# Optimization experiments

Hardware: AMD Instinct MI355X
Metric: run time of the kernel (lower is better)

## Reference

```python
import jax, jax.numpy as jnp
import numpy as np

N_IMAGE, N_CAPTION, N_REGION, N_WORD = 128, 32, 36, 24
EMBED, NUM_BLOCK, N_KERNELS, HID, OUT = 1024, 32, 8, 64, 1
BLOCK = EMBED // NUM_BLOCK  # 32
LAMBDA = 4.0
EPS = 1e-8


def l2norm(x, axis):
    # matches torch l2norm: x / (sqrt(sum(x^2)) + eps)
    return x / (jnp.sqrt(jnp.sum(x * x, axis=axis, keepdims=True)) + EPS)


def wn_linear(x, v, g, b):
    # torch weight_norm(Linear): W = g * v / ||v||_row
    w = v * (g / jnp.linalg.norm(v, axis=1))[:, None]
    return x @ w.T + b


def setup_inputs() -> dict:
    key = jax.random.key(0)
    ks = jax.random.split(key, 12)
    return {
        'images': jax.random.normal(ks[0], (N_IMAGE, N_REGION, EMBED), jnp.float32),
        'captions': jax.random.normal(ks[1], (N_CAPTION, N_WORD, EMBED), jnp.float32),
        'depends': jax.random.randint(ks[2], (N_CAPTION, N_WORD - 1, 2), 0, N_WORD, jnp.int32),
        'cap_lens': jnp.full((N_CAPTION,), N_WORD, jnp.int32),
        'mean_k': jax.random.normal(ks[3], (N_KERNELS,), jnp.float32) * 0.1,
        'prec_k': 1.0 + jax.random.normal(ks[4], (N_KERNELS,), jnp.float32) * 0.1,
        'conv_w': jax.random.normal(ks[5], (N_KERNELS, NUM_BLOCK, HID // N_KERNELS), jnp.float32) * 0.05,
        'out1_v': jax.random.normal(ks[6], (HID, HID), jnp.float32) * 0.05,
        'out1_g': jnp.ones((HID,), jnp.float32),
        'out1_b': jnp.zeros((HID,), jnp.float32),
        'out2_v': jax.random.normal(ks[7], (OUT, HID), jnp.float32) * 0.05,
        'out2_g': jnp.ones((OUT,), jnp.float32),
        'out2_b': jnp.zeros((OUT,), jnp.float32),
    }


def reference(images, captions, depends, cap_lens, mean_k, prec_k, conv_w,
              out1_v, out1_g, out1_b, out2_v, out2_g, out2_b):
    B = images.shape[0]

    def per_caption(cap, dep):
        # cap: (nw, d); dep: (n_dep, 2)
        # --- intra_relations: softmax(Q K^T * lambda) ---
        words_sim = jax.nn.softmax((cap @ cap.T) * LAMBDA, axis=-1)  # (nw, nw)
        # --- build_sparse_graph: symmetric adjacency, pair 0 skipped, + eye ---
        valid = jnp.arange(dep.shape[0]) > 0
        r = jnp.where(valid, dep[:, 0], N_WORD)  # dump invalid into pad row
        c = jnp.where(valid, dep[:, 1], N_WORD)
        adj = jnp.zeros((N_WORD + 1, N_WORD + 1), images.dtype)
        adj = adj.at[r, c].max(1.0)
        adj = adj.at[c, r].max(1.0)
        adj = adj[:N_WORD, :N_WORD] + jnp.eye(N_WORD, dtype=images.dtype)
        # --- node_level_matching: inter_relations + weighted context ---
        attn = jnp.einsum('brd,wd->brw', images, cap)          # (B, R, nw)
        attn = jax.nn.leaky_relu(attn, 0.1)
        attn = l2norm(attn, axis=2)
        attn = jax.nn.softmax(jnp.swapaxes(attn, 1, 2) * LAMBDA, axis=-1)  # (B, nw, R)
        wctx = jnp.einsum('bwr,brd->bwd', attn, images)        # (B, nw, d)
        # block-wise cosine similarity
        q = cap.reshape(N_WORD, NUM_BLOCK, BLOCK)              # (nw, nb, blk)
        ctx = wctx.reshape(B, N_WORD, NUM_BLOCK, BLOCK)        # (B, nw, nb, blk)
        num = jnp.einsum('wkc,nwkc->nwk', q, ctx)
        qn = jnp.linalg.norm(q, axis=-1)                       # (nw, nb)
        cn = jnp.linalg.norm(ctx, axis=-1)                     # (B, nw, nb)
        tnode = num / jnp.maximum(qn[None] * cn, EPS)          # (B, nw, nb)
        # --- structure_level_matching (sparse path) ---
        nb_feat = adj[None, :, :, None] * tnode[:, :, None, :]  # (B, nw, nw, nb)
        nb_w = l2norm(adj * words_sim, axis=1)                  # (nw, nw) neighbor-normalized
        # Gaussian kernel weights of the graph convolution
        diff = (nb_w[..., None] - mean_k) ** 2                  # (nw, nw, nk)
        kw = jnp.exp(-0.5 * diff / (1e-14 + prec_k ** 2))
        kw = kw / jnp.sum(kw, axis=-1, keepdims=True)
        # aggregate neighbors per kernel, then per-kernel linear, concat
        agg = jnp.einsum('ijk,nijf->nikf', kw, nb_feat)         # (B, nw, nk, nb)
        hidden = jnp.einsum('nikf,kfo->niko', agg, conv_w).reshape(B * N_WORD, HID)
        h = jnp.tanh(wn_linear(hidden, out1_v, out1_g, out1_b))
        s = wn_linear(h, out2_v, out2_g, out2_b)                # (B*nw, 1)
        return s.reshape(B, -1).mean(axis=1)                    # (B,)

    sims = jax.vmap(per_caption)(captions, depends)             # (n_caption, B)
    return sims.T                                               # (B, n_caption)
```

## Files before the change

### kernel.cpp

```cpp
#include <hip/hip_runtime.h>
#include <math.h>

#define N_IMAGE   128
#define N_CAPTION 32
#define N_REGION  36
#define N_WORD    24
#define EMBED     1024
#define EPSV      1e-8f

#define WS_W1 0
#define WS_W2 4096
#define WS_S  4160
#define WS_QN 10304

__global__ __launch_bounds__(64) void prep_weights_k(
    const float* __restrict__ v1, const float* __restrict__ g1,
    const float* __restrict__ v2, const float* __restrict__ g2,
    float* __restrict__ ws) {
  const int j = threadIdx.x;
  float s = 0.f;
  for (int c0 = 0; c0 < 64; c0++) { float x = v1[j * 64 + c0]; s += x * x; }
  const float sc = g1[j] / sqrtf(s);
  for (int c0 = 0; c0 < 64; c0++) ws[WS_W1 + j * 64 + c0] = v1[j * 64 + c0] * sc;
  float s2 = 0.f;
  for (int c0 = 0; c0 < 64; c0++) { float x = v2[c0]; s2 += x * x; }
  ws[WS_W2 + j] = v2[j] * (g2[0] / sqrtf(s2));
}

__global__ __launch_bounds__(256) void cap_prep_k(
    const float* __restrict__ captions, const int* __restrict__ depends,
    const float* __restrict__ mean_k, const float* __restrict__ prec_k,
    float* __restrict__ ws) {
  __shared__ __align__(16) float capT[24][132];
  __shared__ float partB[2304];
  __shared__ float wsL[24][25];
  __shared__ float adjL[24][24];

  const int c = blockIdx.x, tid = threadIdx.x;
  const float* capC = captions + c * N_WORD * EMBED;

  const int g = tid / 36, t = tid % 36;
  const int i0 = (t / 6) * 4, j0 = (t % 6) * 4;
  const bool act = tid < 144;
  float acc[4][4] = {};
  for (int k0 = 0; k0 < EMBED; k0 += 128) {
    for (int idx = tid; idx < 24 * 32; idx += 256) {
      int r = idx >> 5, q = idx & 31;
      *(float4*)&capT[r][q * 4] = *(const float4*)(capC + r * EMBED + k0 + q * 4);
    }
    __syncthreads();
    if (act) {
#pragma unroll
      for (int q8 = 0; q8 < 8; q8++) {
        const int q = g * 8 + q8;
        float4 av[4], bv[4];
#pragma unroll
        for (int a = 0; a < 4; a++) av[a] = *(const float4*)&capT[i0 + a][q * 4];
#pragma unroll
        for (int b = 0; b < 4; b++) bv[b] = *(const float4*)&capT[j0 + b][q * 4];
#pragma unroll
        for (int a = 0; a < 4; a++)
#pragma unroll
          for (int b = 0; b < 4; b++)
            acc[a][b] += av[a].x * bv[b].x + av[a].y * bv[b].y +
                         av[a].z * bv[b].z + av[a].w * bv[b].w;
      }
    }
    __syncthreads();
  }
  if (act)
#pragma unroll
    for (int a = 0; a < 4; a++)
#pragma unroll
      for (int b = 0; b < 4; b++)
        partB[g * 576 + (i0 + a) * 24 + (j0 + b)] = acc[a][b];
  __syncthreads();
  for (int p = tid; p < 576; p += 256)
    wsL[p / 24][p % 24] = partB[p] + partB[p + 576] + partB[p + 1152] + partB[p + 1728];
  {
    float* ap = &adjL[0][0];
    for (int p = tid; p < 576; p += 256) ap[p] = 0.f;
  }
  __syncthreads();
  if (tid < 24) {
    const int i = tid;
    float m = -1e30f;
    for (int j = 0; j < 24; j++) m = fmaxf(m, wsL[i][j]);
    float ssum = 0.f;
    for (int j = 0; j < 24; j++) {
      float e = expf(4.0f * (wsL[i][j] - m));
      wsL[i][j] = e; ssum += e;
    }
    float inv = 1.0f / ssum;
    for (int j = 0; j < 24; j++) wsL[i][j] *= inv;
  }
  __syncthreads();
  if (tid >= 1 && tid < 23) {
    int r = depends[c * 46 + tid * 2];
    int cc = depends[c * 46 + tid * 2 + 1];
    if ((unsigned)r < 24u && (unsigned)cc < 24u) {
      adjL[r][cc] = 1.f;
      adjL[cc][r] = 1.f;
    }
  }
  __syncthreads();
  if (tid < 24) adjL[tid][tid] += 1.f;
  __syncthreads();
  if (tid < 24) {
    const int i = tid;
    float mk[8], pk2[8];
#pragma unroll
    for (int k = 0; k < 8; k++) {
      mk[k] = mean_k[k];
      float p = prec_k[k];
      pk2[k] = 1e-14f + p * p;
    }
    float s2 = 0.f;
    for (int j = 0; j < 24; j++) {
      float a = adjL[i][j] * wsL[i][j];
      s2 += a * a;
    }
    const float inv = 1.0f / (sqrtf(s2) + EPSV);
    float accS[8] = {};
    for (int j = 0; j < 24; j++) {
      const float adj_ij = adjL[i][j];
      if (adj_ij != 0.f) {
        const float nb = adj_ij * wsL[i][j] * inv;
        float wk[8], ssum = 0.f;
#pragma unroll
        for (int k = 0; k < 8; k++) {
          float d = nb - mk[k];
          wk[k] = expf(-0.5f * d * d / pk2[k]);
          ssum += wk[k];
        }
        const float invs = adj_ij / ssum;
#pragma unroll
        for (int k = 0; k < 8; k++) accS[k] += wk[k] * invs;
      }
    }
#pragma unroll
    for (int k = 0; k < 8; k++) ws[WS_S + (c * 24 + i) * 8 + k] = accS[k];
  }
  for (int p = tid; p < 768; p += 256) {
    const int w = p >> 5, f = p & 31;
    const float* q = capC + w * EMBED + f * 32;
    float s = 0.f;
#pragma unroll
    for (int d = 0; d < 32; d += 4) {
      float4 v = *(const float4*)(q + d);
      s += v.x * v.x + v.y * v.y + v.z * v.z + v.w * v.w;
    }
    ws[WS_QN + (c * 24 + w) * 32 + f] = sqrtf(s);
  }
}

__global__ __launch_bounds__(256) void main_k(
    const float* __restrict__ images, const float* __restrict__ captions,
    const float* __restrict__ conv_w, const float* __restrict__ out1_b,
    const float* __restrict__ out2_b, const float* __restrict__ ws,
    float* __restrict__ out) {
  __shared__ __align__(16) float imgT[36][132];
  __shared__ __align__(16) float capT[24][132];
  __shared__ float attnL[36][25];
  __shared__ __align__(16) float attnT[36][28];
  __shared__ __align__(16) float ctxL[24][132];
  __shared__ float tnodeL[24][33];
  __shared__ __align__(16) float hiddenL[24][72];
  __shared__ float sred[24];

  const int tid = threadIdx.x;
  const int bid = blockIdx.x;
  const int n = bid >> 5, c = bid & 31;
  const float* imgN = images + n * N_REGION * EMBED;
  const float* capC = captions + c * N_WORD * EMBED;

  const int g1 = tid / 54, t1 = tid % 54;
  const int r0 = (t1 / 6) * 4, w0s1 = (t1 % 6) * 4;
  const bool act1 = tid < 216;
  float acc1[4][4] = {};

  for (int k0 = 0; k0 < EMBED; k0 += 128) {
    for (int idx = tid; idx < 36 * 32; idx += 256) {
      int r = idx >> 5, q = idx & 31;
      *(float4*)&imgT[r][q * 4] = *(const float4*)(imgN + r * EMBED + k0 + q * 4);
    }
    for (int idx = tid; idx < 24 * 32; idx += 256) {
      int r = idx >> 5, q = idx & 31;
      *(float4*)&capT[r][q * 4] = *(const float4*)(capC + r * EMBED + k0 + q * 4);
    }
    __syncthreads();
    if (act1) {
#pragma unroll
      for (int q8 = 0; q8 < 8; q8++) {
        const int q = g1 * 8 + q8;
        float4 av[4], bv[4];
#pragma unroll
        for (int a = 0; a < 4; a++) av[a] = *(const float4*)&imgT[r0 + a][q * 4];
#pragma unroll
        for (int b = 0; b < 4; b++) bv[b] = *(const float4*)&capT[w0s1 + b][q * 4];
#pragma unroll
        for (int a = 0; a < 4; a++)
#pragma unroll
          for (int b = 0; b < 4; b++)
            acc1[a][b] += av[a].x * bv[b].x + av[a].y * bv[b].y +
                          av[a].z * bv[b].z + av[a].w * bv[b].w;
      }
    }
    __syncthreads();
  }
  {
    float* part = &imgT[0][0];
    if (act1) {
#pragma unroll
      for (int a = 0; a < 4; a++)
#pragma unroll
        for (int b = 0; b < 4; b++)
          part[g1 * 864 + (r0 + a) * 24 + (w0s1 + b)] = acc1[a][b];
    }
    __syncthreads();
    for (int p = tid; p < 864; p += 256) {
      float s = part[p] + part[p + 864] + part[p + 1728] + part[p + 2592];
      attnL[p / 24][p % 24] = (s > 0.f) ? s : 0.1f * s;
    }
    __syncthreads();
  }

  if (tid < 36) {
    const int r = tid;
    float s = 0.f;
    for (int w = 0; w < 24; w++) { float x = attnL[r][w]; s += x * x; }
    const float inv = 1.f / (sqrtf(s) + EPSV);
    for (int w = 0; w < 24; w++) attnL[r][w] *= inv;
  }
  __syncthreads();
  if (tid < 24) {
    const int w = tid;
    float m = -1e30f;
    for (int r = 0; r < 36; r++) m = fmaxf(m, attnL[r][w]);
    float ssum = 0.f;
    for (int r = 0; r < 36; r++) {
      float e = expf(4.0f * (attnL[r][w] - m));
      attnT[r][w] = e; ssum += e;
    }
    const float inv = 1.0f / ssum;
    for (int r = 0; r < 36; r++) attnT[r][w] *= inv;
  }
  __syncthreads();

  for (int k0 = 0; k0 < EMBED; k0 += 128) {
    for (int idx = tid; idx < 36 * 32; idx += 256) {
      int r = idx >> 5, q = idx & 31;
      *(float4*)&imgT[r][q * 4] = *(const float4*)(imgN + r * EMBED + k0 + q * 4);
    }
    for (int idx = tid; idx < 24 * 32; idx += 256) {
      int r = idx >> 5, q = idx & 31;
      *(float4*)&capT[r][q * 4] = *(const float4*)(capC + r * EMBED + k0 + q * 4);
    }
    __syncthreads();
    if (tid < 192) {
      const int w0 = (tid >> 5) * 4, dq = tid & 31;
      float4 a0 = make_float4(0.f, 0.f, 0.f, 0.f), a1 = a0, a2 = a0, a3 = a0;
      for (int r = 0; r < 36; r++) {
        float4 iv = *(const float4*)&imgT[r][dq * 4];
        float4 aw = *(const float4*)&attnT[r][w0];
        a0.x += aw.x * iv.x; a0.y += aw.x * iv.y; a0.z += aw.x * iv.z; a0.w += aw.x * iv.w;
        a1.x += aw.y * iv.x; a1.y += aw.y * iv.y; a1.z += aw.y * iv.z; a1.w += aw.y * iv.w;
        a2.x += aw.z * iv.x; a2.y += aw.z * iv.y; a2.z += aw.z * iv.z; a2.w += aw.z * iv.w;
        a3.x += aw.w * iv.x; a3.y += aw.w * iv.y; a3.z += aw.w * iv.z; a3.w += aw.w * iv.w;
      }
      *(float4*)&ctxL[w0 + 0][dq * 4] = a0;
      *(float4*)&ctxL[w0 + 1][dq * 4] = a1;
      *(float4*)&ctxL[w0 + 2][dq * 4] = a2;
      *(float4*)&ctxL[w0 + 3][dq * 4] = a3;
    }
    __syncthreads();
    if (tid < 96) {
      const int w = tid >> 2, fl = tid & 3;
      float num = 0.f, cn2 = 0.f;
#pragma unroll
      for (int d = 0; d < 32; d += 4) {
        float4 cv = *(const float4*)&ctxL[w][fl * 32 + d];
        float4 qv = *(const float4*)&capT[w][fl * 32 + d];
        num += qv.x * cv.x + qv.y * cv.y + qv.z * cv.z + qv.w * cv.w;
        cn2 += cv.x * cv.x + cv.y * cv.y + cv.z * cv.z + cv.w * cv.w;
      }
      const int f = (k0 >> 5) + fl;
      const float qn = ws[WS_QN + (c * 24 + w) * 32 + f];
      tnodeL[w][f] = num / fmaxf(qn * sqrtf(cn2), EPSV);
    }
    __syncthreads();
  }

  float* W1t = &imgT[0][0];
  float* w2s = &capT[0][0];
  float* b1s = &capT[1][0];
  float* Ss  = &attnT[0][0];
  for (int idx = tid; idx < 4096; idx += 256) {
    const int j = idx >> 6, col = idx & 63;
    W1t[col * 68 + j] = ws[WS_W1 + idx];
  }
  for (int p = tid; p < 192; p += 256) Ss[p] = ws[WS_S + c * 192 + p];
  if (tid < 64) w2s[tid] = ws[WS_W2 + tid];
  else if (tid < 128) b1s[tid - 64] = out1_b[tid - 64];
  __syncthreads();

  for (int p = tid; p < 1536; p += 256) {
    const int w = p >> 6, col = p & 63, k = col >> 3, o = col & 7;
    const float* cw = conv_w + k * 256 + o;
    float tacc = 0.f;
#pragma unroll
    for (int f = 0; f < 32; f++) tacc += tnodeL[w][f] * cw[f * 8];
    hiddenL[w][col] = Ss[w * 8 + k] * tacc;
  }
  __syncthreads();

  float hv[2][4];
  {
    int pc = 0;
    for (int p = tid; p < 384; p += 256, pc++) {
      const int w = p >> 4, j0 = (p & 15) * 4;
      float ax = b1s[j0 + 0], ay = b1s[j0 + 1], az = b1s[j0 + 2], aww = b1s[j0 + 3];
      for (int col = 0; col < 64; col += 4) {
        float4 h4 = *(const float4*)&hiddenL[w][col];
        float4 wv0 = *(const float4*)&W1t[(col + 0) * 68 + j0];
        float4 wv1 = *(const float4*)&W1t[(col + 1) * 68 + j0];
        float4 wv2 = *(const float4*)&W1t[(col + 2) * 68 + j0];
        float4 wv3 = *(const float4*)&W1t[(col + 3) * 68 + j0];
        ax  += h4.x * wv0.x + h4.y * wv1.x + h4.z * wv2.x + h4.w * wv3.x;
        ay  += h4.x * wv0.y + h4.y * wv1.y + h4.z * wv2.y + h4.w * wv3.y;
        az  += h4.x * wv0.z + h4.y * wv1.z + h4.z * wv2.z + h4.w * wv3.z;
        aww += h4.x * wv0.w + h4.y * wv1.w + h4.z * wv2.w + h4.w * wv3.w;
      }
      hv[pc][0] = tanhf(ax); hv[pc][1] = tanhf(ay);
      hv[pc][2] = tanhf(az); hv[pc][3] = tanhf(aww);
    }
    __syncthreads();
    pc = 0;
    for (int p = tid; p < 384; p += 256, pc++) {
      const int w = p >> 4, j0 = (p & 15) * 4;
      hiddenL[w][j0 + 0] = hv[pc][0]; hiddenL[w][j0 + 1] = hv[pc][1];
      hiddenL[w][j0 + 2] = hv[pc][2]; hiddenL[w][j0 + 3] = hv[pc][3];
    }
    __syncthreads();
  }

  if (tid < 24) {
    const int w = tid;
    float sv = out2_b[0];
    for (int j = 0; j < 64; j++) sv += hiddenL[w][j] * w2s[j];
    sred[w] = sv;
  }
  __syncthreads();
  if (tid == 0) {
    float s = 0.f;
    for (int w = 0; w < 24; w++) s += sred[w];
    out[n * 32 + c] = s * (1.0f / 24.0f);
  }
}

extern "C" void kernel_launch(void* const* d_in, const int* in_sizes, int n_in,
                              void* d_out, int out_size, void* d_ws, size_t ws_size,
                              hipStream_t stream) {
  const float* images   = (const float*)d_in[0];
  const float* captions = (const float*)d_in[1];
  const int*   depends  = (const int*)d_in[2];
  const float* mean_k   = (const float*)d_in[4];
  const float* prec_k   = (const float*)d_in[5];
  const float* conv_w   = (const float*)d_in[6];
  const float* out1_v   = (const float*)d_in[7];
  const float* out1_g   = (const float*)d_in[8];
  const float* out1_b   = (const float*)d_in[9];
  const float* out2_v   = (const float*)d_in[10];
  const float* out2_g   = (const float*)d_in[11];
  const float* out2_b   = (const float*)d_in[12];
  float* ws  = (float*)d_ws;
  float* out = (float*)d_out;

  prep_weights_k<<<dim3(1), dim3(64), 0, stream>>>(out1_v, out1_g, out2_v, out2_g, ws);
  cap_prep_k<<<dim3(32), dim3(256), 0, stream>>>(captions, depends, mean_k, prec_k, ws);
  main_k<<<dim3(N_IMAGE * N_CAPTION), dim3(256), 0, stream>>>(
      images, captions, conv_w, out1_b, out2_b, ws, out);
}
```

Before: 1.065 ms.

## Shrink main kernel LDS footprint, halve K-chunks, fuse weight prep into cap kernel

```diff
diff --git a/kernel.cpp b/kernel.cpp
--- a/kernel.cpp
+++ b/kernel.cpp
@@ -13,30 +13,37 @@
 #define WS_S  4160
 #define WS_QN 10304
 
-__global__ __launch_bounds__(64) void prep_weights_k(
-    const float* __restrict__ v1, const float* __restrict__ g1,
-    const float* __restrict__ v2, const float* __restrict__ g2,
-    float* __restrict__ ws) {
-  const int j = threadIdx.x;
-  float s = 0.f;
-  for (int c0 = 0; c0 < 64; c0++) { float x = v1[j * 64 + c0]; s += x * x; }
-  const float sc = g1[j] / sqrtf(s);
-  for (int c0 = 0; c0 < 64; c0++) ws[WS_W1 + j * 64 + c0] = v1[j * 64 + c0] * sc;
-  float s2 = 0.f;
-  for (int c0 = 0; c0 < 64; c0++) { float x = v2[c0]; s2 += x * x; }
-  ws[WS_W2 + j] = v2[j] * (g2[0] / sqrtf(s2));
-}
-
 __global__ __launch_bounds__(256) void cap_prep_k(
     const float* __restrict__ captions, const int* __restrict__ depends,
     const float* __restrict__ mean_k, const float* __restrict__ prec_k,
+    const float* __restrict__ v1, const float* __restrict__ g1v,
+    const float* __restrict__ v2, const float* __restrict__ g2v,
     float* __restrict__ ws) {
   __shared__ __align__(16) float capT[24][132];
   __shared__ float partB[2304];
   __shared__ float wsL[24][25];
   __shared__ float adjL[24][24];
 
-  const int c = blockIdx.x, tid = threadIdx.x;
+  const int tid = threadIdx.x;
+
+  if (blockIdx.x == 32) {
+    if (tid < 64) {
+      const int j = tid;
+      float s = 0.f;
+      for (int c0 = 0; c0 < 64; c0 += 4) {
+        float4 x = *(const float4*)(v1 + j * 64 + c0);
+        s += x.x * x.x + x.y * x.y + x.z * x.z + x.w * x.w;
+      }
+      const float sc = g1v[j] / sqrtf(s);
+      for (int c0 = 0; c0 < 64; c0++) ws[WS_W1 + j * 64 + c0] = v1[j * 64 + c0] * sc;
+      float s2 = 0.f;
+      for (int c0 = 0; c0 < 64; c0++) { float x = v2[c0]; s2 += x * x; }
+      ws[WS_W2 + j] = v2[j] * (g2v[0] / sqrtf(s2));
+    }
+    return;
+  }
+
+  const int c = blockIdx.x;
   const float* capC = captions + c * N_WORD * EMBED;
 
   const int g = tid / 36, t = tid % 36;
@@ -154,72 +161,77 @@
   }
 }
 
-__global__ __launch_bounds__(256) void main_k(
+__device__ __forceinline__ void stage_chunk(const float* __restrict__ imgN,
+                                            const float* __restrict__ capC,
+                                            float* IMG, float* CAP,
+                                            int k0, int tid) {
+  for (int idx = tid; idx < 960; idx += 256) {
+    if (idx < 576) {
+      const int r = idx >> 4, q = idx & 15;
+      *(float4*)&IMG[r * 68 + q * 4] = *(const float4*)(imgN + r * EMBED + k0 + q * 4);
+    } else {
+      const int j = idx - 576, r = j >> 4, q = j & 15;
+      *(float4*)&CAP[r * 68 + q * 4] = *(const float4*)(capC + r * EMBED + k0 + q * 4);
+    }
+  }
+}
+
+__global__ __launch_bounds__(256, 4) void main_k(
     const float* __restrict__ images, const float* __restrict__ captions,
     const float* __restrict__ conv_w, const float* __restrict__ out1_b,
     const float* __restrict__ out2_b, const float* __restrict__ ws,
     float* __restrict__ out) {
-  __shared__ __align__(16) float imgT[36][132];
-  __shared__ __align__(16) float capT[24][132];
-  __shared__ float attnL[36][25];
-  __shared__ __align__(16) float attnT[36][28];
-  __shared__ __align__(16) float ctxL[24][132];
-  __shared__ float tnodeL[24][33];
-  __shared__ __align__(16) float hiddenL[24][72];
-  __shared__ float sred[24];
+  __shared__ __align__(16) float bufA[4352];
+  __shared__ __align__(16) float bufB[3648];
+  __shared__ __align__(16) float attnL[36][25];
+  __shared__ float smallb[352];
 
   const int tid = threadIdx.x;
-  const int bid = blockIdx.x;
-  const int n = bid >> 5, c = bid & 31;
+  const int n = blockIdx.x >> 5, c = blockIdx.x & 31;
   const float* imgN = images + n * N_REGION * EMBED;
   const float* capC = captions + c * N_WORD * EMBED;
+  float* IMG = bufA;
+  float* CAP = bufA + 2448;
 
   const int g1 = tid / 54, t1 = tid % 54;
-  const int r0 = (t1 / 6) * 4, w0s1 = (t1 % 6) * 4;
+  const int r0 = (t1 / 6) * 4, w0 = (t1 % 6) * 4;
   const bool act1 = tid < 216;
-  float acc1[4][4] = {};
-
-  for (int k0 = 0; k0 < EMBED; k0 += 128) {
-    for (int idx = tid; idx < 36 * 32; idx += 256) {
-      int r = idx >> 5, q = idx & 31;
-      *(float4*)&imgT[r][q * 4] = *(const float4*)(imgN + r * EMBED + k0 + q * 4);
-    }
-    for (int idx = tid; idx < 24 * 32; idx += 256) {
-      int r = idx >> 5, q = idx & 31;
-      *(float4*)&capT[r][q * 4] = *(const float4*)(capC + r * EMBED + k0 + q * 4);
-    }
+  float acc[4][4] = {};
+  for (int k0 = 0; k0 < EMBED; k0 += 64) {
+    __syncthreads();
+    stage_chunk(imgN, capC, IMG, CAP, k0, tid);
     __syncthreads();
     if (act1) {
 #pragma unroll
-      for (int q8 = 0; q8 < 8; q8++) {
-        const int q = g1 * 8 + q8;
+      for (int qi = 0; qi < 4; qi++) {
+        const int q = g1 * 4 + qi;
         float4 av[4], bv[4];
 #pragma unroll
-        for (int a = 0; a < 4; a++) av[a] = *(const float4*)&imgT[r0 + a][q * 4];
-#pragma unroll
-        for (int b = 0; b < 4; b++) bv[b] = *(const float4*)&capT[w0s1 + b][q * 4];
+        for (int a = 0; a < 4; a++) av[a] = *(const float4*)&IMG[(r0 + a) * 68 + q * 4];
+#pragma unroll
+        for (int b = 0; b < 4; b++) bv[b] = *(const float4*)&CAP[(w0 + b) * 68 + q * 4];
 #pragma unroll
         for (int a = 0; a < 4; a++)
 #pragma unroll
           for (int b = 0; b < 4; b++)
-            acc1[a][b] += av[a].x * bv[b].x + av[a].y * bv[b].y +
-                          av[a].z * bv[b].z + av[a].w * bv[b].w;
-      }
-    }
-    __syncthreads();
-  }
+            acc[a][b] += av[a].x * bv[b].x + av[a].y * bv[b].y +
+                         av[a].z * bv[b].z + av[a].w * bv[b].w;
+      }
+    }
+  }
+  __syncthreads();
   {
-    float* part = &imgT[0][0];
+    float* partB = bufB;
     if (act1) {
 #pragma unroll
       for (int a = 0; a < 4; a++)
 #pragma unroll
         for (int b = 0; b < 4; b++)
-          part[g1 * 864 + (r0 + a) * 24 + (w0s1 + b)] = acc1[a][b];
+          partB[g1 * 864 + (r0 + a) * 24 + (w0 + b)] = acc[a][b];
     }
     __syncthreads();
     for (int p = tid; p < 864; p += 256) {
-      float s = part[p] + part[p + 864] + part[p + 1728] + part[p + 2592];
+      float s = partB[p] + partB[p + 864] + partB[p + 1728] + partB[p + 2592];
       attnL[p / 24][p % 24] = (s > 0.f) ? s : 0.1f * s;
     }
     __syncthreads();
@@ -233,6 +245,7 @@
     for (int w = 0; w < 24; w++) attnL[r][w] *= inv;
   }
   __syncthreads();
+  float* attnW = bufB;
   if (tid < 24) {
     const int w = tid;
     float m = -1e30f;
@@ -240,80 +253,121 @@
     float ssum = 0.f;
     for (int r = 0; r < 36; r++) {
       float e = expf(4.0f * (attnL[r][w] - m));
-      attnT[r][w] = e; ssum += e;
+      attnW[w * 44 + r] = e; ssum += e;
     }
     const float inv = 1.0f / ssum;
-    for (int r = 0; r < 36; r++) attnT[r][w] *= inv;
-  }
-  __syncthreads();
-
-  for (int k0 = 0; k0 < EMBED; k0 += 128) {
-    for (int idx = tid; idx < 36 * 32; idx += 256) {
-      int r = idx >> 5, q = idx & 31;
-      *(float4*)&imgT[r][q * 4] = *(const float4*)(imgN + r * EMBED + k0 + q * 4);
-    }
-    for (int idx = tid; idx < 24 * 32; idx += 256) {
-      int r = idx >> 5, q = idx & 31;
-      *(float4*)&capT[r][q * 4] = *(const float4*)(capC + r * EMBED + k0 + q * 4);
-    }
-    __syncthreads();
-    if (tid < 192) {
-      const int w0 = (tid >> 5) * 4, dq = tid & 31;
-      float4 a0 = make_float4(0.f, 0.f, 0.f, 0.f), a1 = a0, a2 = a0, a3 = a0;
-      for (int r = 0; r < 36; r++) {
-        float4 iv = *(const float4*)&imgT[r][dq * 4];
-        float4 aw = *(const float4*)&attnT[r][w0];
-        a0.x += aw.x * iv.x; a0.y += aw.x * iv.y; a0.z += aw.x * iv.z; a0.w += aw.x * iv.w;
-        a1.x += aw.y * iv.x; a1.y += aw.y * iv.y; a1.z += aw.y * iv.z; a1.w += aw.y * iv.w;
-        a2.x += aw.z * iv.x; a2.y += aw.z * iv.y; a2.z += aw.z * iv.z; a2.w += aw.z * iv.w;
-        a3.x += aw.w * iv.x; a3.y += aw.w * iv.y; a3.z += aw.w * iv.z; a3.w += aw.w * iv.w;
-      }
-      *(float4*)&ctxL[w0 + 0][dq * 4] = a0;
-      *(float4*)&ctxL[w0 + 1][dq * 4] = a1;
-      *(float4*)&ctxL[w0 + 2][dq * 4] = a2;
-      *(float4*)&ctxL[w0 + 3][dq * 4] = a3;
-    }
+    for (int r = 0; r < 36; r++) attnW[w * 44 + r] *= inv;
+  }
+  __syncthreads();
+  float* qnL = &attnL[0][0];
+  for (int p = tid; p < 768; p += 256) qnL[p] = ws[WS_QN + c * 768 + p];
+
+  float* tnodeL = bufB + 1056;
+  const int g3 = tid >> 4, q4 = tid & 15, w03 = g3 * 4;
+  for (int k0 = 0; k0 < EMBED; k0 += 64) {
+    __syncthreads();
+    stage_chunk(imgN, capC, IMG, CAP, k0, tid);
     __syncthreads();
     if (tid < 96) {
-      const int w = tid >> 2, fl = tid & 3;
-      float num = 0.f, cn2 = 0.f;
-#pragma unroll
-      for (int d = 0; d < 32; d += 4) {
-        float4 cv = *(const float4*)&ctxL[w][fl * 32 + d];
-        float4 qv = *(const float4*)&capT[w][fl * 32 + d];
-        num += qv.x * cv.x + qv.y * cv.y + qv.z * cv.z + qv.w * cv.w;
-        cn2 += cv.x * cv.x + cv.y * cv.y + cv.z * cv.z + cv.w * cv.w;
-      }
-      const int f = (k0 >> 5) + fl;
-      const float qn = ws[WS_QN + (c * 24 + w) * 32 + f];
-      tnodeL[w][f] = num / fmaxf(qn * sqrtf(cn2), EPSV);
-    }
-    __syncthreads();
-  }
-
-  float* W1t = &imgT[0][0];
-  float* w2s = &capT[0][0];
-  float* b1s = &capT[1][0];
-  float* Ss  = &attnT[0][0];
+      float4 ctx0 = make_float4(0.f, 0.f, 0.f, 0.f), ctx1 = ctx0, ctx2 = ctx0, ctx3 = ctx0;
+      for (int rb = 0; rb < 36; rb += 4) {
+        float4 iv0 = *(const float4*)&IMG[(rb + 0) * 68 + q4 * 4];
+        float4 iv1 = *(const float4*)&IMG[(rb + 1) * 68 + q4 * 4];
+        float4 iv2 = *(const float4*)&IMG[(rb + 2) * 68 + q4 * 4];
+        float4 iv3 = *(const float4*)&IMG[(rb + 3) * 68 + q4 * 4];
+        float4 a0 = *(const float4*)&attnW[(w03 + 0) * 44 + rb];
+        float4 a1 = *(const float4*)&attnW[(w03 + 1) * 44 + rb];
+        float4 a2 = *(const float4*)&attnW[(w03 + 2) * 44 + rb];
+        float4 a3 = *(const float4*)&attnW[(w03 + 3) * 44 + rb];
+        ctx0.x += a0.x * iv0.x + a0.y * iv1.x + a0.z * iv2.x + a0.w * iv3.x;
+        ctx0.y += a0.x * iv0.y + a0.y * iv1.y + a0.z * iv2.y + a0.w * iv3.y;
+        ctx0.z += a0.x * iv0.z + a0.y * iv1.z + a0.z * iv2.z + a0.w * iv3.z;
+        ctx0.w += a0.x * iv0.w + a0.y * iv1.w + a0.z * iv2.w + a0.w * iv3.w;
+        ctx1.x += a1.x * iv0.x + a1.y * iv1.x + a1.z * iv2.x + a1.w * iv3.x;
+        ctx1.y += a1.x * iv0.y + a1.y * iv1.y + a1.z * iv2.y + a1.w * iv3.y;
+        ctx1.z += a1.x * iv0.z + a1.y * iv1.z + a1.z * iv2.z + a1.w * iv3.z;
+        ctx1.w += a1.x * iv0.w + a1.y * iv1.w + a1.z * iv2.w + a1.w * iv3.w;
+        ctx2.x += a2.x * iv0.x + a2.y * iv1.x + a2.z * iv2.x + a2.w * iv3.x;
+        ctx2.y += a2.x * iv0.y + a2.y * iv1.y + a2.z * iv2.y + a2.w * iv3.y;
+        ctx2.z += a2.x * iv0.z + a2.y * iv1.z + a2.z * iv2.z + a2.w * iv3.z;
+        ctx2.w += a2.x * iv0.w + a2.y * iv1.w + a2.z * iv2.w + a2.w * iv3.w;
+        ctx3.x += a3.x * iv0.x + a3.y * iv1.x + a3.z * iv2.x + a3.w * iv3.x;
+        ctx3.y += a3.x * iv0.y + a3.y * iv1.y + a3.z * iv2.y + a3.w * iv3.y;
+        ctx3.z += a3.x * iv0.z + a3.y * iv1.z + a3.z * iv2.z + a3.w * iv3.z;
+        ctx3.w += a3.x * iv0.w + a3.y * iv1.w + a3.z * iv2.w + a3.w * iv3.w;
+      }
+      float red[8];
+      {
+        float4 c4;
+        c4 = *(const float4*)&CAP[(w03 + 0) * 68 + q4 * 4];
+        red[0] = c4.x * ctx0.x + c4.y * ctx0.y + c4.z * ctx0.z + c4.w * ctx0.w;
+        red[4] = ctx0.x * ctx0.x + ctx0.y * ctx0.y + ctx0.z * ctx0.z + ctx0.w * ctx0.w;
+        c4 = *(const float4*)&CAP[(w03 + 1) * 68 + q4 * 4];
+        red[1] = c4.x * ctx1.x + c4.y * ctx1.y + c4.z * ctx1.z + c4.w * ctx1.w;
+        red[5] = ctx1.x * ctx1.x + ctx1.y * ctx1.y + ctx1.z * ctx1.z + ctx1.w * ctx1.w;
+        c4 = *(const float4*)&CAP[(w03 + 2) * 68 + q4 * 4];
+        red[2] = c4.x * ctx2.x + c4.y * ctx2.y + c4.z * ctx2.z + c4.w * ctx2.w;
+        red[6] = ctx2.x * ctx2.x + ctx2.y * ctx2.y + ctx2.z * ctx2.z + ctx2.w * ctx2.w;
+        c4 = *(const float4*)&CAP[(w03 + 3) * 68 + q4 * 4];
+        red[3] = c4.x * ctx3.x + c4.y * ctx3.y + c4.z * ctx3.z + c4.w * ctx3.w;
+        red[7] = ctx3.x * ctx3.x + ctx3.y * ctx3.y + ctx3.z * ctx3.z + ctx3.w * ctx3.w;
+      }
+#pragma unroll
+      for (int m = 1; m < 8; m <<= 1) {
+#pragma unroll
+        for (int t = 0; t < 8; t++) red[t] += __shfl_xor(red[t], m);
+      }
+      if ((q4 & 7) == 0) {
+        const int f = (k0 >> 5) + (q4 >> 3);
+#pragma unroll
+        for (int j = 0; j < 4; j++) {
+          const float qn = qnL[(w03 + j) * 32 + f];
+          tnodeL[(w03 + j) * 36 + f] = red[j] / fmaxf(qn * sqrtf(red[4 + j]), EPSV);
+        }
+      }
+    }
+  }
+  __syncthreads();
+
+  float* convT = bufA;
+  for (int idx = tid; idx < 2048; idx += 256) {
+    const int f = idx >> 6, col = idx & 63;
+    convT[f * 68 + col] = conv_w[(col >> 3) * 256 + f * 8 + (col & 7)];
+  }
+  float* w2s = smallb, * b1s = smallb + 64, * Ss = smallb + 128, * sred = smallb + 320;
+  for (int p = tid; p < 192; p += 256) Ss[p] = ws[WS_S + c * 192 + p];
+  if (tid < 64) w2s[tid] = ws[WS_W2 + tid];
+  else if (tid < 128) b1s[tid - 64] = out1_b[tid - 64];
+  __syncthreads();
+
+  float* hiddenL = bufB + 1920;
+  {
+    const int col = tid & 63, wg = tid >> 6;
+    float cw[32];
+#pragma unroll
+    for (int f = 0; f < 32; f++) cw[f] = convT[f * 68 + col];
+    const int kk = col >> 3;
+#pragma unroll
+    for (int rnd = 0; rnd < 6; rnd++) {
+      const int w = wg * 6 + rnd;
+      float a = 0.f;
+#pragma unroll
+      for (int f4 = 0; f4 < 8; f4++) {
+        float4 t4 = *(const float4*)&tnodeL[w * 36 + f4 * 4];
+        a += t4.x * cw[f4 * 4 + 0] + t4.y * cw[f4 * 4 + 1] +
+             t4.z * cw[f4 * 4 + 2] + t4.w * cw[f4 * 4 + 3];
+      }
+      hiddenL[w * 72 + col] = Ss[w * 8 + kk] * a;
+    }
+  }
+  __syncthreads();
+
+  float* W1t = bufA;
   for (int idx = tid; idx < 4096; idx += 256) {
     const int j = idx >> 6, col = idx & 63;
     W1t[col * 68 + j] = ws[WS_W1 + idx];
   }
-  for (int p = tid; p < 192; p += 256) Ss[p] = ws[WS_S + c * 192 + p];
-  if (tid < 64) w2s[tid] = ws[WS_W2 + tid];
-  else if (tid < 128) b1s[tid - 64] = out1_b[tid - 64];
-  __syncthreads();
-
-  for (int p = tid; p < 1536; p += 256) {
-    const int w = p >> 6, col = p & 63, k = col >> 3, o = col & 7;
-    const float* cw = conv_w + k * 256 + o;
-    float tacc = 0.f;
-#pragma unroll
-    for (int f = 0; f < 32; f++) tacc += tnodeL[w][f] * cw[f * 8];
-    hiddenL[w][col] = Ss[w * 8 + k] * tacc;
-  }
-  __syncthreads();
-
+  __syncthreads();
   float hv[2][4];
   {
     int pc = 0;
@@ -321,7 +375,7 @@
       const int w = p >> 4, j0 = (p & 15) * 4;
       float ax = b1s[j0 + 0], ay = b1s[j0 + 1], az = b1s[j0 + 2], aww = b1s[j0 + 3];
       for (int col = 0; col < 64; col += 4) {
-        float4 h4 = *(const float4*)&hiddenL[w][col];
+        float4 h4 = *(const float4*)&hiddenL[w * 72 + col];
         float4 wv0 = *(const float4*)&W1t[(col + 0) * 68 + j0];
         float4 wv1 = *(const float4*)&W1t[(col + 1) * 68 + j0];
         float4 wv2 = *(const float4*)&W1t[(col + 2) * 68 + j0];
@@ -338,8 +392,8 @@
     pc = 0;
     for (int p = tid; p < 384; p += 256, pc++) {
       const int w = p >> 4, j0 = (p & 15) * 4;
-      hiddenL[w][j0 + 0] = hv[pc][0]; hiddenL[w][j0 + 1] = hv[pc][1];
-      hiddenL[w][j0 + 2] = hv[pc][2]; hiddenL[w][j0 + 3] = hv[pc][3];
+      hiddenL[w * 72 + j0 + 0] = hv[pc][0]; hiddenL[w * 72 + j0 + 1] = hv[pc][1];
+      hiddenL[w * 72 + j0 + 2] = hv[pc][2]; hiddenL[w * 72 + j0 + 3] = hv[pc][3];
     }
     __syncthreads();
   }
@@ -347,7 +401,7 @@
   if (tid < 24) {
     const int w = tid;
     float sv = out2_b[0];
-    for (int j = 0; j < 64; j++) sv += hiddenL[w][j] * w2s[j];
+    for (int j = 0; j < 64; j++) sv += hiddenL[w * 72 + j] * w2s[j];
     sred[w] = sv;
   }
   __syncthreads();
@@ -376,8 +430,8 @@
   float* ws  = (float*)d_ws;
   float* out = (float*)d_out;
 
-  prep_weights_k<<<dim3(1), dim3(64), 0, stream>>>(out1_v, out1_g, out2_v, out2_g, ws);
-  cap_prep_k<<<dim3(32), dim3(256), 0, stream>>>(captions, depends, mean_k, prec_k, ws);
+  cap_prep_k<<<dim3(33), dim3(256), 0, stream>>>(
+      captions, depends, mean_k, prec_k, out1_v, out1_g, out2_v, out2_g, ws);
   main_k<<<dim3(N_IMAGE * N_CAPTION), dim3(256), 0, stream>>>(
       images, captions, conv_w, out1_b, out2_b, ws, out);
 }
```

Measured after the change: 1.511 ms. 41.9% more time.
